# Kernel optimization log

Hardware: AMD Instinct MI355X
Metric: run time of the kernel (lower is better)

## Reference

```python
import jax, jax.numpy as jnp
import numpy as np

NEG_ATT = 0.2   # GATv2Conv internal leaky_relu slope
NEG_ACT = 0.01  # nn.LeakyReLU default slope (activation between layers)

def _segment_softmax(logits, seg, n):
    m = jax.ops.segment_max(logits, seg, num_segments=n)
    ex = jnp.exp(logits - m[seg])
    s = jax.ops.segment_sum(ex, seg, num_segments=n)
    return ex / s[seg]

def _gatv2(h, Wl, bl, Wr, br, att, bias, src, dst, n):
    # PyG GATv2Conv, heads=1: xl = lin_l(h) (source/message), xr = lin_r(h) (target)
    xl = h @ Wl + bl                                   # [N, H]
    xr = h @ Wr + br                                   # [N, H]
    e = jax.nn.leaky_relu(xl[src] + xr[dst], NEG_ATT)  # [E, H]
    logits = e @ att                                   # [E]
    alpha = _segment_softmax(logits, dst, n)           # softmax over incoming edges per dst
    out = jax.ops.segment_sum(xl[src] * alpha[:, None], dst, num_segments=n)
    return out + bias

def setup_inputs() -> dict:
    key = jax.random.key(0)
    G, P, DEG, DIN, H, EX, OUT, NC = 4096, 24, 8, 32, 128, 8, 3, 6
    N = G * P
    E = N * DEG
    ks = jax.random.split(key, 16)
    x = jax.random.normal(ks[0], (N, DIN), jnp.float32)
    gid = jnp.arange(E) // (P * DEG)  # edges stay within their graph
    src = gid * P + jax.random.randint(ks[1], (E,), 0, P)
    dst = gid * P + jax.random.randint(ks[2], (E,), 0, P)
    batch = jnp.repeat(jnp.arange(G), P)
    extra_feat = jax.random.normal(ks[3], (G, EX), jnp.float32)
    sc = lambda k, shp: jax.random.normal(k, shp, jnp.float32) * 0.05
    return dict(
        x=x, src=src, dst=dst, batch=batch, extra_feat=extra_feat,
        W_init0=sc(ks[4], (DIN, H)), b_init0=jnp.zeros((H,), jnp.float32),
        W_init1=sc(ks[5], (H, H)), b_init1=jnp.zeros((H,), jnp.float32),
        Wl=sc(ks[6], (NC, H, H)), bl=jnp.zeros((NC, H), jnp.float32),
        Wr=sc(ks[7], (NC, H, H)), br=jnp.zeros((NC, H), jnp.float32),
        att=sc(ks[8], (NC, H)), cbias=jnp.zeros((NC, H), jnp.float32),
        Wf0=sc(ks[9], (H + EX, H)), bf0=jnp.zeros((H,), jnp.float32),
        Wf1=sc(ks[10], (H, H)), bf1=jnp.zeros((H,), jnp.float32),
        Wf2=sc(ks[11], (H, OUT)), bf2=jnp.zeros((OUT,), jnp.float32),
    )

def reference(x, src, dst, batch, extra_feat,
              W_init0, b_init0, W_init1, b_init1,
              Wl, bl, Wr, br, att, cbias,
              Wf0, bf0, Wf1, bf1, Wf2, bf2):
    N = x.shape[0]
    G = extra_feat.shape[0]
    # init MLP
    h = jax.nn.leaky_relu(x @ W_init0 + b_init0, NEG_ACT)
    h = jax.nn.leaky_relu(h @ W_init1 + b_init1, NEG_ACT)
    # GATv2Conv adds self-loops
    loop = jnp.arange(N)
    src_sl = jnp.concatenate([src, loop])
    dst_sl = jnp.concatenate([dst, loop])
    NUM_GAT, MP = 2, 3
    for g in range(NUM_GAT):
        for m in range(MP):
            c = g * MP + m
            h = _gatv2(h, Wl[c], bl[c], Wr[c], br[c], att[c], cbias[c], src_sl, dst_sl, N)
            if m < MP - 1:  # BasicGNN: act between convs, not after last
                h = jax.nn.leaky_relu(h, NEG_ACT)
    # global_add_pool + extra features + final MLP
    pooled = jax.ops.segment_sum(h, batch, num_segments=G)
    z = jnp.concatenate([pooled, extra_feat], axis=1)
    z = jax.nn.leaky_relu(z @ Wf0 + bf0, NEG_ACT)
    z = jax.nn.leaky_relu(z @ Wf1 + bf1, NEG_ACT)
    return z @ Wf2 + bf2
```

## Files before the change

### kernel.cpp

```cpp
#include <hip/hip_runtime.h>

#define NG   4096
#define P    24
#define EPG  192
#define ESL  216
#define DIN  32
#define H    128
#define EX   8
#define NOUT 3
#define HSS  136
#define XTS  40

typedef short bf16x8 __attribute__((ext_vector_type(8)));
typedef float f32x4  __attribute__((ext_vector_type(4)));

__device__ __forceinline__ float u2f(unsigned u) { return __uint_as_float(u); }
__device__ __forceinline__ unsigned short f2bf(float v) {
    unsigned u = __float_as_uint(v);
    unsigned r = u + 0x7fffu + ((u >> 16) & 1u);
    return (unsigned short)(r >> 16);
}
__device__ __forceinline__ float lrelu(float v, float s) { return v > 0.f ? v : v * s; }

__global__ void cvtw(const float* __restrict__ W0, const float* __restrict__ W1,
                     const float* __restrict__ Wl, const float* __restrict__ Wr,
                     unsigned short* __restrict__ ws) {
    int i = blockIdx.x * 256 + threadIdx.x;
    float v;
    if (i < 4096)            { int n = i >> 5, k = i & 31;  v = W0[k * 128 + n]; }
    else if (i < 20480)      { int j = i - 4096;  int n = j >> 7, k = j & 127; v = W1[k * 128 + n]; }
    else if (i < 118784)     { int j = i - 20480; int c = j >> 14, r = j & 16383;
                               int n = r >> 7, k = r & 127; v = Wl[c * 16384 + k * 128 + n]; }
    else if (i < 217088)     { int j = i - 118784; int c = j >> 14, r = j & 16383;
                               int n = r >> 7, k = r & 127; v = Wr[c * 16384 + k * 128 + n]; }
    else return;
    ws[i] = f2bf(v);
}

#define EDGE_PAIR(wa, wb, p, q)                                   \
    do {                                                          \
        float a0_ = u2f((wa) << 16);                              \
        float a1_ = u2f((wa) & 0xffff0000u);                      \
        float b0_ = u2f((wb) << 16);                              \
        float b1_ = u2f((wb) & 0xffff0000u);                      \
        abss = fmaf(fabsf(a0_ + b0_), (p), abss);                 \
        abss = fmaf(fabsf(a1_ + b1_), (q), abss);                 \
    } while (0)

#define DOT_PAIR(wv, p, q)                                        \
    do {                                                          \
        sum = fmaf(u2f((wv) << 16), (p), sum);                    \
        sum = fmaf(u2f((wv) & 0xffff0000u), (q), sum);            \
    } while (0)

__global__ __launch_bounds__(256, 4) void gat_all(
    const float* __restrict__ x,
    const int*   __restrict__ src,
    const int*   __restrict__ dst,
    const float* __restrict__ extra,
    const float* __restrict__ b0,  const float* __restrict__ b1,
    const float* __restrict__ bl,  const float* __restrict__ br,
    const float* __restrict__ att, const float* __restrict__ cbias,
    const float* __restrict__ Wf0, const float* __restrict__ bf0,
    const float* __restrict__ Wf1, const float* __restrict__ bf1,
    const float* __restrict__ Wf2, const float* __restrict__ bf2,
    const unsigned short* __restrict__ wsb,
    float* __restrict__ out)
{
    __shared__ __align__(16) unsigned short hb [32 * HSS];
    __shared__ __align__(16) unsigned short xlb[32 * HSS];
    __shared__ __align__(16) unsigned short xrb[32 * HSS];
    __shared__ __align__(16) unsigned short xlT[128 * XTS];
    __shared__ __align__(16) float          Am[1024];
    __shared__ __align__(16) float          att_s[H];

    float* dsum = Am + 768;
    float* slr  = Am + 792;

    const int g    = blockIdx.x;
    const int t    = threadIdx.x;
    const int lane = t & 63;
    const int w    = t >> 6;
    const int m16  = lane & 15;
    const int kc   = lane >> 4;
    const long long gn = (long long)g * P;

    const unsigned short* W0T = wsb;
    const unsigned short* W1T = wsb + 4096;
    const unsigned short* WLT = wsb + 20480;
    const unsigned short* WRT = wsb + 118784;

    int s_e = 0, d_e = 0;
    if (t < ESL) {
        if (t < EPG) {
            s_e = src[(long long)g * EPG + t] - (int)gn;
            d_e = dst[(long long)g * EPG + t] - (int)gn;
        } else { s_e = d_e = t - EPG; }
    }

    if (t < 192) {
        float4 v = *reinterpret_cast<const float4*>(&x[gn * DIN + t * 4]);
        int n = t >> 3, k = (t & 7) * 4;
        *reinterpret_cast<ushort4*>(&xlT[n * XTS + k]) =
            make_ushort4(f2bf(v.x), f2bf(v.y), f2bf(v.z), f2bf(v.w));
    } else {
        int u = t - 192;
        int r = 24 + (u >> 3), k = (u & 7) * 4;
        *reinterpret_cast<ushort4*>(&xlT[r * XTS + k]) = make_ushort4(0, 0, 0, 0);
    }
    __syncthreads();

    {
        f32x4 acc[4] = {};
        bf16x8 a = *reinterpret_cast<const bf16x8*>(&xlT[((w & 1) * 16 + m16) * XTS + kc * 8]);
        #pragma unroll
        for (int i = 0; i < 4; ++i) {
            int nt = (w >> 1) * 4 + i;
            bf16x8 b = *reinterpret_cast<const bf16x8*>(&W0T[(nt * 16 + m16) * 32 + kc * 8]);
            acc[i] = __builtin_amdgcn_mfma_f32_16x16x32_bf16(a, b, acc[i], 0, 0, 0);
        }
        #pragma unroll
        for (int i = 0; i < 4; ++i) {
            int col = (w >> 1) * 64 + i * 16 + m16;
            float bv = b0[col];
            #pragma unroll
            for (int r = 0; r < 4; ++r) {
                int row = (w & 1) * 16 + kc * 4 + r;
                xlb[row * HSS + col] = f2bf(lrelu(acc[i][r] + bv, 0.01f));
            }
        }
    }
    __syncthreads();

    {
        f32x4 acc[4] = {};
        for (int kt = 0; kt < 4; ++kt) {
            bf16x8 a = *reinterpret_cast<const bf16x8*>(&xlb[((w & 1) * 16 + m16) * HSS + kt * 32 + kc * 8]);
            #pragma unroll
            for (int i = 0; i < 4; ++i) {
                int nt = (w >> 1) * 4 + i;
                bf16x8 b = *reinterpret_cast<const bf16x8*>(&W1T[(nt * 16 + m16) * 128 + kt * 32 + kc * 8]);
                acc[i] = __builtin_amdgcn_mfma_f32_16x16x32_bf16(a, b, acc[i], 0, 0, 0);
            }
        }
        #pragma unroll
        for (int i = 0; i < 4; ++i) {
            int col = (w >> 1) * 64 + i * 16 + m16;
            float bv = b1[col];
            #pragma unroll
            for (int r = 0; r < 4; ++r) {
                int row = (w & 1) * 16 + kc * 4 + r;
                hb[row * HSS + col] = f2bf(lrelu(acc[i][r] + bv, 0.01f));
            }
        }
    }
    __syncthreads();

    for (int c = 0; c < 6; ++c) {
        if (t < H)   att_s[t] = att[c * H + t];
        if (t < 192) *reinterpret_cast<float4*>(&Am[t * 4]) = make_float4(0.f, 0.f, 0.f, 0.f);
        if (t < P)   dsum[t] = 0.f;

        const unsigned short* WT   = ((w & 1) ? WRT : WLT) + c * 16384;
        const float*          bias = ((w & 1) ? br : bl) + c * H;
        f32x4 acc[8] = {};
        for (int kt = 0; kt < 4; ++kt) {
            bf16x8 a0 = *reinterpret_cast<const bf16x8*>(&hb[(m16)      * HSS + kt * 32 + kc * 8]);
            bf16x8 a1 = *reinterpret_cast<const bf16x8*>(&hb[(16 + m16) * HSS + kt * 32 + kc * 8]);
            #pragma unroll
            for (int i = 0; i < 4; ++i) {
                int nt = (w >> 1) * 4 + i;
                bf16x8 b = *reinterpret_cast<const bf16x8*>(&WT[(nt * 16 + m16) * 128 + kt * 32 + kc * 8]);
                acc[i]     = __builtin_amdgcn_mfma_f32_16x16x32_bf16(a0, b, acc[i],     0, 0, 0);
                acc[4 + i] = __builtin_amdgcn_mfma_f32_16x16x32_bf16(a1, b, acc[4 + i], 0, 0, 0);
            }
        }
        {
            unsigned short* XO = (w & 1) ? xrb : xlb;
            const bool isL = !(w & 1);
            #pragma unroll
            for (int mt = 0; mt < 2; ++mt)
            #pragma unroll
            for (int i = 0; i < 4; ++i) {
                int col = (w >> 1) * 64 + i * 16 + m16;
                float bv = bias[col];
                unsigned short ub[4];
                #pragma unroll
                for (int r = 0; r < 4; ++r) {
                    int row = mt * 16 + kc * 4 + r;
                    ub[r] = f2bf(acc[mt * 4 + i][r] + bv);
                    XO[row * HSS + col] = ub[r];
                }
                if (isL)
                    *reinterpret_cast<ushort4*>(&xlT[col * XTS + mt * 16 + kc * 4]) =
                        make_ushort4(ub[0], ub[1], ub[2], ub[3]);
            }
        }
        __syncthreads();

        float abss = 0.f;
        if (t < ESL) {
            const uint4*  xa = reinterpret_cast<const uint4*>(&xlb[s_e * HSS]);
            const uint4*  xb = reinterpret_cast<const uint4*>(&xrb[d_e * HSS]);
            const float4* ap = reinterpret_cast<const float4*>(att_s);
            #pragma unroll 4
            for (int cc = 0; cc < 16; ++cc) {
                uint4 wa = xa[cc], wb = xb[cc];
                float4 p0 = ap[cc * 2], p1 = ap[cc * 2 + 1];
                EDGE_PAIR(wa.x, wb.x, p0.x, p0.y);
                EDGE_PAIR(wa.y, wb.y, p0.z, p0.w);
                EDGE_PAIR(wa.z, wb.z, p1.x, p1.y);
                EDGE_PAIR(wa.w, wb.w, p1.z, p1.w);
            }
        } else {
            int u = t - ESL;
            const float4* ap = reinterpret_cast<const float4*>(att_s);
            for (int task = u; task < 48; task += 40) {
                int node = task >> 1;
                const uint4* rp = reinterpret_cast<const uint4*>(
                    ((task & 1) ? xrb : xlb) + node * HSS);
                float sum = 0.f;
                #pragma unroll 4
                for (int cc = 0; cc < 16; ++cc) {
                    uint4 wv = rp[cc];
                    float4 p0 = ap[cc * 2], p1 = ap[cc * 2 + 1];
                    DOT_PAIR(wv.x, p0.x, p0.y);
                    DOT_PAIR(wv.y, p0.z, p0.w);
                    DOT_PAIR(wv.z, p1.x, p1.y);
                    DOT_PAIR(wv.w, p1.z, p1.w);
                }
                slr[task] = sum;
            }
        }
        __syncthreads();

        float ex = 0.f;
        if (t < ESL) {
            float lg = 0.4f * abss + 0.6f * (slr[2 * s_e] + slr[2 * d_e + 1]);
            ex = __expf(lg);
            atomicAdd(&dsum[d_e], ex);
        }
        __syncthreads();
        if (t < ESL) atomicAdd(&Am[d_e * 32 + s_e], ex / dsum[d_e]);
        __syncthreads();

        {
            int arow = (w & 1) * 16 + m16;
            float4 u0 = *reinterpret_cast<const float4*>(&Am[arow * 32 + kc * 8]);
            float4 u1 = *reinterpret_cast<const float4*>(&Am[arow * 32 + kc * 8 + 4]);
            bf16x8 a;
            a[0] = (short)f2bf(u0.x); a[1] = (short)f2bf(u0.y);
            a[2] = (short)f2bf(u0.z); a[3] = (short)f2bf(u0.w);
            a[4] = (short)f2bf(u1.x); a[5] = (short)f2bf(u1.y);
            a[6] = (short)f2bf(u1.z); a[7] = (short)f2bf(u1.w);
            f32x4 acc2[4] = {};
            #pragma unroll
            for (int i = 0; i < 4; ++i) {
                int nt = (w >> 1) * 4 + i;
                bf16x8 b = *reinterpret_cast<const bf16x8*>(&xlT[(nt * 16 + m16) * XTS + kc * 8]);
                acc2[i] = __builtin_amdgcn_mfma_f32_16x16x32_bf16(a, b, acc2[i], 0, 0, 0);
            }
            const bool doact = (c % 3) < 2;
            #pragma unroll
            for (int i = 0; i < 4; ++i) {
                int col = (w >> 1) * 64 + i * 16 + m16;
                float cb = cbias[c * H + col];
                #pragma unroll
                for (int r = 0; r < 4; ++r) {
                    int row = (w & 1) * 16 + kc * 4 + r;
                    float v = acc2[i][r] + cb;
                    if (doact) v = lrelu(v, 0.01f);
                    hb[row * HSS + col] = f2bf(v);
                }
            }
        }
        __syncthreads();
    }

    float* z  = Am;
    float* pa = Am + 144;
    float* pb = Am + 288;
    float* h1 = Am + 432;
    float* qa = Am + 576;
    float* qb = Am + 720;
    float* h2 = Am + 864;
    if (t < H) {
        float s = 0.f;
        for (int r = 0; r < P; ++r) s += u2f(((unsigned)hb[r * HSS + t]) << 16);
        z[t] = s;
    } else if (t < H + EX) {
        z[t] = extra[(long long)g * EX + (t - H)];
    }
    __syncthreads();
    {
        int j = t & 127, half = t >> 7;
        float a = half ? 0.f : bf0[j];
        int k0 = half ? 68 : 0, k1 = half ? 136 : 68;
        for (int k = k0; k < k1; ++k) a += z[k] * Wf0[k * H + j];
        (half ? pb : pa)[j] = a;
    }
    __syncthreads();
    if (t < H) h1[t] = lrelu(pa[t] + pb[t], 0.01f);
    __syncthreads();
    {
        int j = t & 127, half = t >> 7;
        float a = half ? 0.f : bf1[j];
        int k0 = half * 64, k1 = k0 + 64;
        for (int k = k0; k < k1; ++k) a += h1[k] * Wf1[k * H + j];
        (half ? qb : qa)[j] = a;
    }
    __syncthreads();
    if (t < H) h2[t] = lrelu(qa[t] + qb[t], 0.01f);
    __syncthreads();
    if (t < NOUT) {
        float a = bf2[t];
        for (int k = 0; k < H; ++k) a += h2[k] * Wf2[k * NOUT + t];
        out[(long long)g * NOUT + t] = a;
    }
}

extern "C" void kernel_launch(void* const* d_in, const int* in_sizes, int n_in,
                              void* d_out, int out_size, void* d_ws, size_t ws_size,
                              hipStream_t stream) {
    (void)in_sizes; (void)n_in; (void)out_size; (void)ws_size;
    const float* x     = (const float*)d_in[0];
    const int*   src   = (const int*)  d_in[1];
    const int*   dst   = (const int*)  d_in[2];
    const float* extra = (const float*)d_in[4];
    const float* W0    = (const float*)d_in[5];
    const float* b0    = (const float*)d_in[6];
    const float* W1    = (const float*)d_in[7];
    const float* b1    = (const float*)d_in[8];
    const float* Wl    = (const float*)d_in[9];
    const float* bl    = (const float*)d_in[10];
    const float* Wr    = (const float*)d_in[11];
    const float* br    = (const float*)d_in[12];
    const float* att   = (const float*)d_in[13];
    const float* cbias = (const float*)d_in[14];
    const float* Wf0   = (const float*)d_in[15];
    const float* bf0   = (const float*)d_in[16];
    const float* Wf1   = (const float*)d_in[17];
    const float* bf1   = (const float*)d_in[18];
    const float* Wf2   = (const float*)d_in[19];
    const float* bf2   = (const float*)d_in[20];
    unsigned short* wsb = (unsigned short*)d_ws;
    float* out = (float*)d_out;

    cvtw<<<848, 256, 0, stream>>>(W0, W1, Wl, Wr, wsb);
    gat_all<<<NG, 256, 0, stream>>>(x, src, dst, extra, b0, b1, bl, br, att, cbias,
                                    Wf0, bf0, Wf1, bf1, Wf2, bf2, wsb, out);
}
```

Before: 394.6 us.

## Switch to fp16 MFMA, fold attention projections into GEMM, defer softmax normalization

Changes all bf16 storage and MFMA to fp16, which enables packed half adds and v_dot2_f32_f16 for the per-edge |xl+xr|·att reduction. The per-node linear attention terms (xl·att, xr·att) are precomputed as W·att vectors in the weight conversion kernel and computed as an extra MFMA column inside the node GEMM, replacing a separate dot-product pass and one barrier. Softmax normalization is deferred: unnormalized exps are accumulated into the adjacency matrix and the per-row reciprocal of the sum is applied after aggregation, which removes another barrier. fp16 has less range than bf16, so overflow is a risk if activations grow, and exp is not max-shifted.

Result: faster. 369.9 us (-6.3%).

```diff
diff --git a/kernel.cpp b/kernel.cpp
--- a/kernel.cpp
+++ b/kernel.cpp
@@ -9,49 +9,57 @@
 #define EX   8
 #define NOUT 3
 #define HSS  136
-#define XTS  40
-
-typedef short bf16x8 __attribute__((ext_vector_type(8)));
-typedef float f32x4  __attribute__((ext_vector_type(4)));
-
-__device__ __forceinline__ float u2f(unsigned u) { return __uint_as_float(u); }
-__device__ __forceinline__ unsigned short f2bf(float v) {
-    unsigned u = __float_as_uint(v);
-    unsigned r = u + 0x7fffu + ((u >> 16) & 1u);
-    return (unsigned short)(r >> 16);
+#define XTS  36
+
+typedef _Float16 f16x8 __attribute__((ext_vector_type(8)));
+typedef _Float16 h2    __attribute__((ext_vector_type(2)));
+typedef float    f32x4 __attribute__((ext_vector_type(4)));
+
+__device__ __forceinline__ unsigned short f2h(float v) {
+    _Float16 h = (_Float16)v; unsigned short u; __builtin_memcpy(&u, &h, 2); return u;
+}
+__device__ __forceinline__ float h2f(unsigned short u) {
+    _Float16 h; __builtin_memcpy(&h, &u, 2); return (float)h;
+}
+__device__ __forceinline__ unsigned pkadd(unsigned a, unsigned b) {
+    h2 x, y; __builtin_memcpy(&x, &a, 4); __builtin_memcpy(&y, &b, 4);
+    h2 z = x + y; unsigned r; __builtin_memcpy(&r, &z, 4); return r;
 }
 __device__ __forceinline__ float lrelu(float v, float s) { return v > 0.f ? v : v * s; }
 
 __global__ void cvtw(const float* __restrict__ W0, const float* __restrict__ W1,
                      const float* __restrict__ Wl, const float* __restrict__ Wr,
-                     unsigned short* __restrict__ ws) {
+                     const float* __restrict__ att, const float* __restrict__ bl,
+                     const float* __restrict__ br, unsigned short* __restrict__ ws) {
     int i = blockIdx.x * 256 + threadIdx.x;
-    float v;
-    if (i < 4096)            { int n = i >> 5, k = i & 31;  v = W0[k * 128 + n]; }
-    else if (i < 20480)      { int j = i - 4096;  int n = j >> 7, k = j & 127; v = W1[k * 128 + n]; }
-    else if (i < 118784)     { int j = i - 20480; int c = j >> 14, r = j & 16383;
+    if (i < 217088) {
+        float v;
+        if (i < 4096)        { int n = i >> 5, k = i & 31;  v = W0[k * 128 + n]; }
+        else if (i < 20480)  { int j = i - 4096;  int n = j >> 7, k = j & 127; v = W1[k * 128 + n]; }
+        else if (i < 118784) { int j = i - 20480; int c = j >> 14, r = j & 16383;
                                int n = r >> 7, k = r & 127; v = Wl[c * 16384 + k * 128 + n]; }
-    else if (i < 217088)     { int j = i - 118784; int c = j >> 14, r = j & 16383;
+        else                 { int j = i - 118784; int c = j >> 14, r = j & 16383;
                                int n = r >> 7, k = r & 127; v = Wr[c * 16384 + k * 128 + n]; }
-    else return;
-    ws[i] = f2bf(v);
-}
-
-#define EDGE_PAIR(wa, wb, p, q)                                   \
-    do {                                                          \
-        float a0_ = u2f((wa) << 16);                              \
-        float a1_ = u2f((wa) & 0xffff0000u);                      \
-        float b0_ = u2f((wb) << 16);                              \
-        float b1_ = u2f((wb) & 0xffff0000u);                      \
-        abss = fmaf(fabsf(a0_ + b0_), (p), abss);                 \
-        abss = fmaf(fabsf(a1_ + b1_), (q), abss);                 \
-    } while (0)
-
-#define DOT_PAIR(wv, p, q)                                        \
-    do {                                                          \
-        sum = fmaf(u2f((wv) << 16), (p), sum);                    \
-        sum = fmaf(u2f((wv) & 0xffff0000u), (q), sum);            \
-    } while (0)
+        ws[i] = f2h(v);
+    } else if (i < 241664) {
+        int j = i - 217088;
+        const float* W = (j < 12288) ? Wl : Wr;
+        if (j >= 12288) j -= 12288;
+        int c = j >> 11, r = j & 2047, row = r >> 7, k = r & 127;
+        float v = 0.f;
+        if (row == 0) {
+            for (int q = 0; q < 128; ++q) v += W[c * 16384 + k * 128 + q] * att[c * 128 + q];
+        }
+        ws[i] = f2h(v);
+    } else if (i < 241676) {
+        int c = i - 241664;
+        const float* B = (c < 6) ? bl : br;
+        int cc = (c < 6) ? c : c - 6;
+        float s = 0.f;
+        for (int q = 0; q < 128; ++q) s += B[cc * 128 + q] * att[cc * 128 + q];
+        ((float*)(ws + 241664))[c] = s;
+    }
+}
 
 __global__ __launch_bounds__(256, 4) void gat_all(
     const float* __restrict__ x,
@@ -72,10 +80,9 @@
     __shared__ __align__(16) unsigned short xrb[32 * HSS];
     __shared__ __align__(16) unsigned short xlT[128 * XTS];
     __shared__ __align__(16) float          Am[1024];
-    __shared__ __align__(16) float          att_s[H];
-
-    float* dsum = Am + 768;
-    float* slr  = Am + 792;
+    __shared__ __align__(16) unsigned int   att_h[64];
+    __shared__ float dsum[32];
+    __shared__ float snode[64];
 
     const int g    = blockIdx.x;
     const int t    = threadIdx.x;
@@ -89,6 +96,7 @@
     const unsigned short* W1T = wsb + 4096;
     const unsigned short* WLT = wsb + 20480;
     const unsigned short* WRT = wsb + 118784;
+    const float* wsf = (const float*)(wsb + 241664);
 
     int s_e = 0, d_e = 0;
     if (t < ESL) {
@@ -102,7 +110,7 @@
         float4 v = *reinterpret_cast<const float4*>(&x[gn * DIN + t * 4]);
         int n = t >> 3, k = (t & 7) * 4;
         *reinterpret_cast<ushort4*>(&xlT[n * XTS + k]) =
-            make_ushort4(f2bf(v.x), f2bf(v.y), f2bf(v.z), f2bf(v.w));
+            make_ushort4(f2h(v.x), f2h(v.y), f2h(v.z), f2h(v.w));
     } else {
         int u = t - 192;
         int r = 24 + (u >> 3), k = (u & 7) * 4;
@@ -112,12 +120,12 @@
 
     {
         f32x4 acc[4] = {};
-        bf16x8 a = *reinterpret_cast<const bf16x8*>(&xlT[((w & 1) * 16 + m16) * XTS + kc * 8]);
+        f16x8 a = *reinterpret_cast<const f16x8*>(&xlT[((w & 1) * 16 + m16) * XTS + kc * 8]);
         #pragma unroll
         for (int i = 0; i < 4; ++i) {
             int nt = (w >> 1) * 4 + i;
-            bf16x8 b = *reinterpret_cast<const bf16x8*>(&W0T[(nt * 16 + m16) * 32 + kc * 8]);
-            acc[i] = __builtin_amdgcn_mfma_f32_16x16x32_bf16(a, b, acc[i], 0, 0, 0);
+            f16x8 b = *reinterpret_cast<const f16x8*>(&W0T[(nt * 16 + m16) * 32 + kc * 8]);
+            acc[i] = __builtin_amdgcn_mfma_f32_16x16x32_f16(a, b, acc[i], 0, 0, 0);
         }
         #pragma unroll
         for (int i = 0; i < 4; ++i) {
@@ -126,7 +134,7 @@
             #pragma unroll
             for (int r = 0; r < 4; ++r) {
                 int row = (w & 1) * 16 + kc * 4 + r;
-                xlb[row * HSS + col] = f2bf(lrelu(acc[i][r] + bv, 0.01f));
+                xlb[row * HSS + col] = f2h(lrelu(acc[i][r] + bv, 0.01f));
             }
         }
     }
@@ -135,12 +143,12 @@
     {
         f32x4 acc[4] = {};
         for (int kt = 0; kt < 4; ++kt) {
-            bf16x8 a = *reinterpret_cast<const bf16x8*>(&xlb[((w & 1) * 16 + m16) * HSS + kt * 32 + kc * 8]);
+            f16x8 a = *reinterpret_cast<const f16x8*>(&xlb[((w & 1) * 16 + m16) * HSS + kt * 32 + kc * 8]);
             #pragma unroll
             for (int i = 0; i < 4; ++i) {
                 int nt = (w >> 1) * 4 + i;
-                bf16x8 b = *reinterpret_cast<const bf16x8*>(&W1T[(nt * 16 + m16) * 128 + kt * 32 + kc * 8]);
-                acc[i] = __builtin_amdgcn_mfma_f32_16x16x32_bf16(a, b, acc[i], 0, 0, 0);
+                f16x8 b = *reinterpret_cast<const f16x8*>(&W1T[(nt * 16 + m16) * 128 + kt * 32 + kc * 8]);
+                acc[i] = __builtin_amdgcn_mfma_f32_16x16x32_f16(a, b, acc[i], 0, 0, 0);
             }
         }
         #pragma unroll
@@ -150,29 +158,37 @@
             #pragma unroll
             for (int r = 0; r < 4; ++r) {
                 int row = (w & 1) * 16 + kc * 4 + r;
-                hb[row * HSS + col] = f2bf(lrelu(acc[i][r] + bv, 0.01f));
+                hb[row * HSS + col] = f2h(lrelu(acc[i][r] + bv, 0.01f));
             }
         }
     }
     __syncthreads();
 
     for (int c = 0; c < 6; ++c) {
-        if (t < H)   att_s[t] = att[c * H + t];
-        if (t < 192) *reinterpret_cast<float4*>(&Am[t * 4]) = make_float4(0.f, 0.f, 0.f, 0.f);
-        if (t < P)   dsum[t] = 0.f;
+        *reinterpret_cast<float4*>(&Am[t * 4]) = make_float4(0.f, 0.f, 0.f, 0.f);
+        if (t < 32) dsum[t] = (t < P) ? 0.f : 1.0f;
+        if (t < 64) att_h[t] = ((unsigned)f2h(att[c * H + 2 * t])) |
+                               (((unsigned)f2h(att[c * H + 2 * t + 1])) << 16);
 
         const unsigned short* WT   = ((w & 1) ? WRT : WLT) + c * 16384;
+        const unsigned short* WAX  = wsb + 217088 + ((w & 1) ? 12288 : 0) + c * 2048;
         const float*          bias = ((w & 1) ? br : bl) + c * H;
         f32x4 acc[8] = {};
+        f32x4 acce[2] = {};
         for (int kt = 0; kt < 4; ++kt) {
-            bf16x8 a0 = *reinterpret_cast<const bf16x8*>(&hb[(m16)      * HSS + kt * 32 + kc * 8]);
-            bf16x8 a1 = *reinterpret_cast<const bf16x8*>(&hb[(16 + m16) * HSS + kt * 32 + kc * 8]);
+            f16x8 a0 = *reinterpret_cast<const f16x8*>(&hb[(m16)      * HSS + kt * 32 + kc * 8]);
+            f16x8 a1 = *reinterpret_cast<const f16x8*>(&hb[(16 + m16) * HSS + kt * 32 + kc * 8]);
             #pragma unroll
             for (int i = 0; i < 4; ++i) {
                 int nt = (w >> 1) * 4 + i;
-                bf16x8 b = *reinterpret_cast<const bf16x8*>(&WT[(nt * 16 + m16) * 128 + kt * 32 + kc * 8]);
-                acc[i]     = __builtin_amdgcn_mfma_f32_16x16x32_bf16(a0, b, acc[i],     0, 0, 0);
-                acc[4 + i] = __builtin_amdgcn_mfma_f32_16x16x32_bf16(a1, b, acc[4 + i], 0, 0, 0);
+                f16x8 b = *reinterpret_cast<const f16x8*>(&WT[(nt * 16 + m16) * 128 + kt * 32 + kc * 8]);
+                acc[i]     = __builtin_amdgcn_mfma_f32_16x16x32_f16(a0, b, acc[i],     0, 0, 0);
+                acc[4 + i] = __builtin_amdgcn_mfma_f32_16x16x32_f16(a1, b, acc[4 + i], 0, 0, 0);
+            }
+            if (w >= 2) {
+                f16x8 bx = *reinterpret_cast<const f16x8*>(&WAX[m16 * 128 + kt * 32 + kc * 8]);
+                acce[0] = __builtin_amdgcn_mfma_f32_16x16x32_f16(a0, bx, acce[0], 0, 0, 0);
+                acce[1] = __builtin_amdgcn_mfma_f32_16x16x32_f16(a1, bx, acce[1], 0, 0, 0);
             }
         }
         {
@@ -188,78 +204,70 @@
                 #pragma unroll
                 for (int r = 0; r < 4; ++r) {
                     int row = mt * 16 + kc * 4 + r;
-                    ub[r] = f2bf(acc[mt * 4 + i][r] + bv);
+                    ub[r] = f2h(acc[mt * 4 + i][r] + bv);
                     XO[row * HSS + col] = ub[r];
                 }
                 if (isL)
                     *reinterpret_cast<ushort4*>(&xlT[col * XTS + mt * 16 + kc * 4]) =
                         make_ushort4(ub[0], ub[1], ub[2], ub[3]);
             }
+            if (w >= 2 && m16 == 0) {
+                float cst = (w == 2) ? wsf[c] : wsf[6 + c];
+                float* dp = (w == 2) ? snode : (snode + 32);
+                #pragma unroll
+                for (int mt = 0; mt < 2; ++mt)
+                #pragma unroll
+                for (int r = 0; r < 4; ++r)
+                    dp[mt * 16 + kc * 4 + r] = acce[mt][r] + cst;
+            }
         }
         __syncthreads();
 
-        float abss = 0.f;
         if (t < ESL) {
-            const uint4*  xa = reinterpret_cast<const uint4*>(&xlb[s_e * HSS]);
-            const uint4*  xb = reinterpret_cast<const uint4*>(&xrb[d_e * HSS]);
-            const float4* ap = reinterpret_cast<const float4*>(att_s);
+            const uint4* xa = reinterpret_cast<const uint4*>(&xlb[s_e * HSS]);
+            const uint4* xb = reinterpret_cast<const uint4*>(&xrb[d_e * HSS]);
+            const uint4* ap = reinterpret_cast<const uint4*>(att_h);
+            float a0 = 0.f, a1 = 0.f, a2 = 0.f, a3 = 0.f;
             #pragma unroll 4
             for (int cc = 0; cc < 16; ++cc) {
-                uint4 wa = xa[cc], wb = xb[cc];
-                float4 p0 = ap[cc * 2], p1 = ap[cc * 2 + 1];
-                EDGE_PAIR(wa.x, wb.x, p0.x, p0.y);
-                EDGE_PAIR(wa.y, wb.y, p0.z, p0.w);
-                EDGE_PAIR(wa.z, wb.z, p1.x, p1.y);
-                EDGE_PAIR(wa.w, wb.w, p1.z, p1.w);
-            }
-        } else {
-            int u = t - ESL;
-            const float4* ap = reinterpret_cast<const float4*>(att_s);
-            for (int task = u; task < 48; task += 40) {
-                int node = task >> 1;
-                const uint4* rp = reinterpret_cast<const uint4*>(
-                    ((task & 1) ? xrb : xlb) + node * HSS);
-                float sum = 0.f;
-                #pragma unroll 4
-                for (int cc = 0; cc < 16; ++cc) {
-                    uint4 wv = rp[cc];
-                    float4 p0 = ap[cc * 2], p1 = ap[cc * 2 + 1];
-                    DOT_PAIR(wv.x, p0.x, p0.y);
-                    DOT_PAIR(wv.y, p0.z, p0.w);
-                    DOT_PAIR(wv.z, p1.x, p1.y);
-                    DOT_PAIR(wv.w, p1.z, p1.w);
-                }
-                slr[task] = sum;
-            }
-        }
-        __syncthreads();
-
-        float ex = 0.f;
-        if (t < ESL) {
-            float lg = 0.4f * abss + 0.6f * (slr[2 * s_e] + slr[2 * d_e + 1]);
-            ex = __expf(lg);
+                uint4 wa = xa[cc], wb = xb[cc], pp = ap[cc];
+                unsigned u0 = pkadd(wa.x, wb.x) & 0x7fff7fffu;
+                unsigned u1 = pkadd(wa.y, wb.y) & 0x7fff7fffu;
+                unsigned u2 = pkadd(wa.z, wb.z) & 0x7fff7fffu;
+                unsigned u3 = pkadd(wa.w, wb.w) & 0x7fff7fffu;
+                asm volatile("v_dot2_f32_f16 %0, %1, %2, %0" : "+v"(a0) : "v"(u0), "v"(pp.x));
+                asm volatile("v_dot2_f32_f16 %0, %1, %2, %0" : "+v"(a1) : "v"(u1), "v"(pp.y));
+                asm volatile("v_dot2_f32_f16 %0, %1, %2, %0" : "+v"(a2) : "v"(u2), "v"(pp.z));
+                asm volatile("v_dot2_f32_f16 %0, %1, %2, %0" : "+v"(a3) : "v"(u3), "v"(pp.w));
+            }
+            float abss = (a0 + a1) + (a2 + a3);
+            float lg = fmaf(0.6f, snode[s_e] + snode[32 + d_e], 0.4f * abss);
+            float ex = __expf(lg);
+            atomicAdd(&Am[d_e * 32 + s_e], ex);
             atomicAdd(&dsum[d_e], ex);
         }
-        __syncthreads();
-        if (t < ESL) atomicAdd(&Am[d_e * 32 + s_e], ex / dsum[d_e]);
         __syncthreads();
 
         {
             int arow = (w & 1) * 16 + m16;
             float4 u0 = *reinterpret_cast<const float4*>(&Am[arow * 32 + kc * 8]);
             float4 u1 = *reinterpret_cast<const float4*>(&Am[arow * 32 + kc * 8 + 4]);
-            bf16x8 a;
-            a[0] = (short)f2bf(u0.x); a[1] = (short)f2bf(u0.y);
-            a[2] = (short)f2bf(u0.z); a[3] = (short)f2bf(u0.w);
-            a[4] = (short)f2bf(u1.x); a[5] = (short)f2bf(u1.y);
-            a[6] = (short)f2bf(u1.z); a[7] = (short)f2bf(u1.w);
+            f16x8 a;
+            a[0] = (_Float16)u0.x; a[1] = (_Float16)u0.y;
+            a[2] = (_Float16)u0.z; a[3] = (_Float16)u0.w;
+            a[4] = (_Float16)u1.x; a[5] = (_Float16)u1.y;
+            a[6] = (_Float16)u1.z; a[7] = (_Float16)u1.w;
             f32x4 acc2[4] = {};
             #pragma unroll
             for (int i = 0; i < 4; ++i) {
                 int nt = (w >> 1) * 4 + i;
-                bf16x8 b = *reinterpret_cast<const bf16x8*>(&xlT[(nt * 16 + m16) * XTS + kc * 8]);
-                acc2[i] = __builtin_amdgcn_mfma_f32_16x16x32_bf16(a, b, acc2[i], 0, 0, 0);
-            }
+                f16x8 b = *reinterpret_cast<const f16x8*>(&xlT[(nt * 16 + m16) * XTS + kc * 8]);
+                acc2[i] = __builtin_amdgcn_mfma_f32_16x16x32_f16(a, b, acc2[i], 0, 0, 0);
+            }
+            float inv[4];
+            #pragma unroll
+            for (int r = 0; r < 4; ++r)
+                inv[r] = __builtin_amdgcn_rcpf(dsum[(w & 1) * 16 + kc * 4 + r]);
             const bool doact = (c % 3) < 2;
             #pragma unroll
             for (int i = 0; i < 4; ++i) {
@@ -268,9 +276,9 @@
                 #pragma unroll
                 for (int r = 0; r < 4; ++r) {
                     int row = (w & 1) * 16 + kc * 4 + r;
-                    float v = acc2[i][r] + cb;
+                    float v = fmaf(acc2[i][r], inv[r], cb);
                     if (doact) v = lrelu(v, 0.01f);
-                    hb[row * HSS + col] = f2bf(v);
+                    hb[row * HSS + col] = f2h(v);
                 }
             }
         }
@@ -286,7 +294,7 @@
     float* h2 = Am + 864;
     if (t < H) {
         float s = 0.f;
-        for (int r = 0; r < P; ++r) s += u2f(((unsigned)hb[r * HSS + t]) << 16);
+        for (int r = 0; r < P; ++r) s += h2f(hb[r * HSS + t]);
         z[t] = s;
     } else if (t < H + EX) {
         z[t] = extra[(long long)g * EX + (t - H)];
@@ -346,7 +354,7 @@
     unsigned short* wsb = (unsigned short*)d_ws;
     float* out = (float*)d_out;
 
-    cvtw<<<848, 256, 0, stream>>>(W0, W1, Wl, Wr, wsb);
+    cvtw<<<945, 256, 0, stream>>>(W0, W1, Wl, Wr, att, bl, br, wsb);
     gat_all<<<NG, 256, 0, stream>>>(x, src, dst, extra, b0, b1, bl, br, att, cbias,
                                     Wf0, bf0, Wf1, bf1, Wf2, bf2, wsb, out);
 }
```
